# Optimization experiments

Hardware: AMD Instinct MI355X
Metric: run time of the kernel (lower is better)

Reference implementation:

```python
import jax, jax.numpy as jnp
import numpy as np

PRESERVE_RATIO = 0.8
TEMPERATURE = 1.5


def setup_inputs() -> dict:
    key = jax.random.key(0)
    ks = jax.random.split(key, 8)
    B, C, H, W = 2, 64, 96, 96
    inter = C // 2
    bott = C // 4
    s = 0.02
    return {
        "x": jax.random.normal(ks[0], (B, C, H, W), dtype=jnp.float32),
        "g_w": jax.random.normal(ks[1], (inter, C), dtype=jnp.float32) * s,
        "theta_w": jax.random.normal(ks[2], (inter, C), dtype=jnp.float32) * s,
        "phi_w": jax.random.normal(ks[3], (inter, C), dtype=jnp.float32) * s,
        "W_w": jax.random.normal(ks[4], (C, inter), dtype=jnp.float32) * s,
        "cg1_w": jax.random.normal(ks[5], (bott, C), dtype=jnp.float32) * s,
        "cg1_b": jnp.zeros((bott,), dtype=jnp.float32),
        "cg2_w": jax.random.normal(ks[6], (C, bott), dtype=jnp.float32) * s,
        "cg2_b": jnp.zeros((C,), dtype=jnp.float32),
    }


def reference(x, g_w, theta_w, phi_w, W_w, cg1_w, cg1_b, cg2_w, cg2_b):
    B, C, H, W = x.shape
    N = H * W
    # color gate: global avg pool -> 1x1 conv -> relu -> 1x1 conv -> sigmoid
    pooled = jnp.mean(x, axis=(2, 3))                       # [B, C]
    h = jax.nn.relu(pooled @ cg1_w.T + cg1_b)               # [B, C//4]
    gate = jax.nn.sigmoid(h @ cg2_w.T + cg2_b)              # [B, C]

    xf = x.reshape(B, C, N)                                 # [B, C, N]
    g_x = jnp.einsum('ic,bcn->bni', g_w, xf)                # [B, N, I]
    theta = jnp.einsum('ic,bcn->bni', theta_w, xf)          # [B, N, I]
    phi = jnp.einsum('ic,bcn->bin', phi_w, xf)              # [B, I, N]

    affinity = jnp.einsum('bni,bim->bnm', theta, phi) / TEMPERATURE  # [B, N, N]
    affinity = jax.nn.softmax(affinity, axis=-1)
    y = jnp.einsum('bnm,bmi->bni', affinity, g_x)           # [B, N, I]
    y = jnp.einsum('ci,bni->bcn', W_w, y).reshape(B, C, H, W)
    y = y * gate[:, :, None, None] * PRESERVE_RATIO
    return x + y
```

## Files before the change

kernel.cpp:

```cpp
#include <hip/hip_runtime.h>

#define N_TOK 9216
#define C_DIM 64
#define I_DIM 32
#define BOT 16
#define B_SZ 2
#define N_TILES 144

typedef short bf16x8 __attribute__((ext_vector_type(8)));
typedef float f32x4 __attribute__((ext_vector_type(4)));
typedef float f32x16 __attribute__((ext_vector_type(16)));

__device__ __forceinline__ unsigned packbf(float a, float b) {
  return __builtin_amdgcn_perm(__float_as_uint(b), __float_as_uint(a), 0x07060302u);
}
__device__ __forceinline__ unsigned short bftrunc(float f) {
  return (unsigned short)(__float_as_uint(f) >> 16);
}

__global__ __launch_bounds__(256) void pool_kernel(const float* __restrict__ x,
                                                   float* __restrict__ pooled) {
  int bc = blockIdx.x;
  const float* p = x + (size_t)bc * N_TOK;
  float s = 0.f;
  for (int t = threadIdx.x; t < N_TOK; t += 256) s += p[t];
#pragma unroll
  for (int off = 32; off >= 1; off >>= 1) s += __shfl_down(s, off, 64);
  __shared__ float red[4];
  int wid = threadIdx.x >> 6, lane = threadIdx.x & 63;
  if (lane == 0) red[wid] = s;
  __syncthreads();
  if (threadIdx.x == 0)
    pooled[bc] = (red[0] + red[1] + red[2] + red[3]) * (1.0f / N_TOK);
}

__global__ __launch_bounds__(256) void proj_kernel(
    const float* __restrict__ x, const float* __restrict__ g_w,
    const float* __restrict__ theta_w, const float* __restrict__ phi_w,
    unsigned short* __restrict__ Q, unsigned short* __restrict__ K,
    unsigned short* __restrict__ VT) {
  const int lane = threadIdx.x & 63;
  const int m = lane & 15, quad = lane >> 4;
  int task = blockIdx.x * 4 + (threadIdx.x >> 6);
  int mat = task / 1152;
  int r0 = task % 1152;
  int b = r0 / 576;
  int n0 = (r0 % 576) * 16;
  const float* wsrc = (mat == 0) ? theta_w : ((mat == 1) ? phi_w : g_w);
  const float scale = (mat == 0) ? 0.96179669439f : 1.0f;

  bf16x8 afr[2][2];
#pragma unroll
  for (int it = 0; it < 2; ++it)
#pragma unroll
    for (int cs = 0; cs < 2; ++cs) {
      const float* wp = wsrc + (it * 16 + m) * C_DIM + cs * 32 + quad * 8;
      union { unsigned u[4]; bf16x8 v; } t;
#pragma unroll
      for (int j = 0; j < 4; ++j)
        t.u[j] = packbf(wp[2 * j] * scale, wp[2 * j + 1] * scale);
      afr[it][cs] = t.v;
    }

  const float* xb = x + (size_t)b * C_DIM * N_TOK + n0 + m;
  bf16x8 bfr[2];
#pragma unroll
  for (int cs = 0; cs < 2; ++cs) {
    union { unsigned u[4]; bf16x8 v; } t;
#pragma unroll
    for (int j = 0; j < 4; ++j) {
      float v0 = xb[(size_t)(cs * 32 + quad * 8 + 2 * j) * N_TOK];
      float v1 = xb[(size_t)(cs * 32 + quad * 8 + 2 * j + 1) * N_TOK];
      t.u[j] = packbf(v0, v1);
    }
    bfr[cs] = t.v;
  }

  f32x4 acc[2] = {{0.f, 0.f, 0.f, 0.f}, {0.f, 0.f, 0.f, 0.f}};
#pragma unroll
  for (int cs = 0; cs < 2; ++cs)
#pragma unroll
    for (int it = 0; it < 2; ++it)
      acc[it] = __builtin_amdgcn_mfma_f32_16x16x32_bf16(afr[it][cs], bfr[cs],
                                                        acc[it], 0, 0, 0);
  if (mat < 2) {
    unsigned short* dst =
        ((mat == 0) ? Q : K) + ((size_t)b * N_TOK + n0 + m) * I_DIM;
#pragma unroll
    for (int it = 0; it < 2; ++it) {
      unsigned u0 = packbf(acc[it][0], acc[it][1]);
      unsigned u1 = packbf(acc[it][2], acc[it][3]);
      *(uint2*)(dst + it * 16 + quad * 4) = make_uint2(u0, u1);
    }
  } else {
#pragma unroll
    for (int it = 0; it < 2; ++it)
#pragma unroll
      for (int r = 0; r < 4; ++r)
        VT[((size_t)b * I_DIM + it * 16 + quad * 4 + r) * N_TOK + n0 + m] =
            bftrunc(acc[it][r]);
  }
}

__global__ __launch_bounds__(256, 4) void attn_kernel(
    const unsigned short* __restrict__ Q, const unsigned short* __restrict__ Kg,
    const unsigned short* __restrict__ VT, float* __restrict__ Ypart,
    float* __restrict__ Lpart, int tps) {
  const int lane = threadIdx.x & 63;
  const int l32 = lane & 31, h = lane >> 5;
  const int wid = threadIdx.x >> 6;
  const int qw = blockIdx.x * 4 + wid;
  const int ks = blockIdx.y, b = blockIdx.z;
  const int q0 = qw * 32;
  const unsigned short* Qb = Q + (size_t)b * N_TOK * I_DIM;
  const unsigned short* Kb = Kg + (size_t)b * N_TOK * I_DIM;
  const unsigned short* Vb = VT + (size_t)b * I_DIM * N_TOK;

  __shared__ __align__(16) unsigned short Pw[4][32][68];
  unsigned short(*P)[68] = Pw[wid];

  bf16x8 bq0 = *(const bf16x8*)(Qb + (size_t)(q0 + l32) * I_DIM + h * 8);
  bf16x8 bq1 = *(const bf16x8*)(Qb + (size_t)(q0 + l32) * I_DIM + 16 + h * 8);

  const f32x16 zz = {};
  f32x16 accy = {};
  float lsum = 0.f;

  const int kt0 = ks * tps;
  for (int kt = kt0; kt < kt0 + tps; ++kt) {
    const int k0 = kt * 64;
    const unsigned short* kp = Kb + (size_t)(k0 + l32) * I_DIM + h * 8;
    bf16x8 ak00 = *(const bf16x8*)(kp);
    bf16x8 ak01 = *(const bf16x8*)(kp + 16);
    bf16x8 ak10 = *(const bf16x8*)(kp + 32 * I_DIM);
    bf16x8 ak11 = *(const bf16x8*)(kp + 32 * I_DIM + 16);
    const unsigned short* vp = Vb + (size_t)l32 * N_TOK + k0 + h * 8;
    bf16x8 bv[4];
    bv[0] = *(const bf16x8*)(vp);
    bv[1] = *(const bf16x8*)(vp + 16);
    bv[2] = *(const bf16x8*)(vp + 32);
    bv[3] = *(const bf16x8*)(vp + 48);

    f32x16 s0 = __builtin_amdgcn_mfma_f32_32x32x16_bf16(ak00, bq0, zz, 0, 0, 0);
    s0 = __builtin_amdgcn_mfma_f32_32x32x16_bf16(ak01, bq1, s0, 0, 0, 0);
    f32x16 s1 = __builtin_amdgcn_mfma_f32_32x32x16_bf16(ak10, bq0, zz, 0, 0, 0);
    s1 = __builtin_amdgcn_mfma_f32_32x32x16_bf16(ak11, bq1, s1, 0, 0, 0);

#pragma unroll
    for (int t = 0; t < 2; ++t) {
      const f32x16 sv = t ? s1 : s0;
      float e[16];
#pragma unroll
      for (int r = 0; r < 16; ++r) {
        e[r] = __builtin_amdgcn_exp2f(sv[r]);
        lsum += e[r];
      }
      unsigned pk[8];
#pragma unroll
      for (int i = 0; i < 8; ++i) pk[i] = packbf(e[2 * i], e[2 * i + 1]);
      unsigned short* row = &P[l32][t * 32 + 4 * h];
      *(uint2*)(row) = make_uint2(pk[0], pk[1]);
      *(uint2*)(row + 8) = make_uint2(pk[2], pk[3]);
      *(uint2*)(row + 16) = make_uint2(pk[4], pk[5]);
      *(uint2*)(row + 24) = make_uint2(pk[6], pk[7]);
    }

#pragma unroll
    for (int s = 0; s < 4; ++s) {
      union { uint2 d[2]; bf16x8 v; } ap;
      const unsigned short* rp = &P[l32][16 * s + 8 * h];
      ap.d[0] = *(const uint2*)(rp);
      ap.d[1] = *(const uint2*)(rp + 4);
      accy = __builtin_amdgcn_mfma_f32_32x32x16_bf16(ap.v, bv[s], accy, 0, 0, 0);
    }
  }

  lsum += __shfl_xor(lsum, 32, 64);

  const size_t base = (size_t)(ks * B_SZ + b) * N_TOK + q0;
#pragma unroll
  for (int R = 0; R < 4; ++R)
#pragma unroll
    for (int r = 0; r < 4; ++r)
      Ypart[(base + r + 8 * R + 4 * h) * I_DIM + l32] = accy[4 * R + r];
  if (h == 0) Lpart[base + l32] = lsum;
}

__global__ __launch_bounds__(256) void epilogue_kernel(
    const float* __restrict__ x, const float* __restrict__ W_w,
    const float* __restrict__ pooled, const float* __restrict__ cg1_w,
    const float* __restrict__ cg1_b, const float* __restrict__ cg2_w,
    const float* __restrict__ cg2_b, const float* __restrict__ Ypart,
    const float* __restrict__ Lpart, float* __restrict__ out, int KS) {
  __shared__ float Ysh[64][33];
  __shared__ float lsh[64];
  __shared__ float gsh[64];
  __shared__ float hl[BOT];
  const int t = threadIdx.x;
  const int b = blockIdx.y;
  const int n0 = blockIdx.x * 64;

  if (t < BOT) {
    float a = cg1_b[t];
#pragma unroll
    for (int c = 0; c < C_DIM; ++c)
      a += cg1_w[t * C_DIM + c] * pooled[b * C_DIM + c];
    hl[t] = a > 0.f ? a : 0.f;
  }

  {
    int nl = t >> 2, i0 = (t & 3) * 8;
    float4 s0 = make_float4(0.f, 0.f, 0.f, 0.f), s1 = s0;
    for (int ks = 0; ks < KS; ++ks) {
      const float* yp =
          Ypart + ((size_t)(ks * B_SZ + b) * N_TOK + n0 + nl) * I_DIM + i0;
      float4 v0 = *(const float4*)(yp);
      float4 v1 = *(const float4*)(yp + 4);
      s0.x += v0.x; s0.y += v0.y; s0.z += v0.z; s0.w += v0.w;
      s1.x += v1.x; s1.y += v1.y; s1.z += v1.z; s1.w += v1.w;
    }
    Ysh[nl][i0 + 0] = s0.x; Ysh[nl][i0 + 1] = s0.y;
    Ysh[nl][i0 + 2] = s0.z; Ysh[nl][i0 + 3] = s0.w;
    Ysh[nl][i0 + 4] = s1.x; Ysh[nl][i0 + 5] = s1.y;
    Ysh[nl][i0 + 6] = s1.z; Ysh[nl][i0 + 7] = s1.w;
    if (t < 64) {
      float ls = 0.f;
      for (int ks = 0; ks < KS; ++ks)
        ls += Lpart[(size_t)(ks * B_SZ + b) * N_TOK + n0 + t];
      lsh[t] = ls;
    }
  }
  __syncthreads();

  if (t < C_DIM) {
    float z = cg2_b[t];
#pragma unroll
    for (int j = 0; j < BOT; ++j) z += cg2_w[t * BOT + j] * hl[j];
    gsh[t] = 0.8f / (1.f + __expf(-z));
  }
  __syncthreads();

  const int n = t & 63, cg = t >> 6;
  float y[I_DIM];
#pragma unroll
  for (int i = 0; i < I_DIM; ++i) y[i] = Ysh[n][i];
  const float inv = 1.0f / lsh[n];
  const float* xb = x + ((size_t)b * C_DIM + cg * 16) * N_TOK + n0 + n;
  float* ob = out + ((size_t)b * C_DIM + cg * 16) * N_TOK + n0 + n;
#pragma unroll
  for (int c16 = 0; c16 < 16; ++c16) {
    const int c = cg * 16 + c16;
    float sacc = 0.f;
#pragma unroll
    for (int i = 0; i < I_DIM; ++i) sacc += W_w[c * I_DIM + i] * y[i];
    ob[(size_t)c16 * N_TOK] = xb[(size_t)c16 * N_TOK] + gsh[c] * inv * sacc;
  }
}

extern "C" void kernel_launch(void* const* d_in, const int* in_sizes, int n_in,
                              void* d_out, int out_size, void* d_ws, size_t ws_size,
                              hipStream_t stream) {
  const float* x = (const float*)d_in[0];
  const float* g_w = (const float*)d_in[1];
  const float* theta_w = (const float*)d_in[2];
  const float* phi_w = (const float*)d_in[3];
  const float* W_w = (const float*)d_in[4];
  const float* cg1_w = (const float*)d_in[5];
  const float* cg1_b = (const float*)d_in[6];
  const float* cg2_w = (const float*)d_in[7];
  const float* cg2_b = (const float*)d_in[8];
  float* out = (float*)d_out;

  char* w = (char*)d_ws;
  const size_t bfsz = (size_t)B_SZ * N_TOK * I_DIM * sizeof(unsigned short);
  unsigned short* Qb = (unsigned short*)(w);
  unsigned short* Kb = (unsigned short*)(w + bfsz);
  unsigned short* VT = (unsigned short*)(w + 2 * bfsz);
  float* pooled = (float*)(w + 3 * bfsz);
  char* w2 = w + 3 * bfsz + 1024;

  int KS = 8;
  {
    const size_t per = (size_t)B_SZ * N_TOK * sizeof(float) * (I_DIM + 1);
    while (KS > 1 && (3 * bfsz + 1024 + (size_t)KS * per) > ws_size) KS >>= 1;
  }
  float* Lpart = (float*)w2;
  float* Ypart = (float*)(w2 + (size_t)KS * B_SZ * N_TOK * sizeof(float));
  int tps = N_TILES / KS;

  proj_kernel<<<dim3(864), 256, 0, stream>>>(x, g_w, theta_w, phi_w, Qb, Kb, VT);
  pool_kernel<<<dim3(B_SZ * C_DIM), 256, 0, stream>>>(x, pooled);
  attn_kernel<<<dim3(72, KS, B_SZ), 256, 0, stream>>>(Qb, Kb, VT, Ypart, Lpart, tps);
  epilogue_kernel<<<dim3(N_TOK / 64, B_SZ), 256, 0, stream>>>(
      x, W_w, pooled, cg1_w, cg1_b, cg2_w, cg2_b, Ypart, Lpart, out, KS);
}
```

Before: 173.6 us.

## Fuse pooling into projection, raise split-K and occupancy, transpose Ypart layout

Merges the pooling kernel into the projection kernel as extra blocks, which removes one launch. Raises attention occupancy hints from 4 to 8 waves and the key split from 8 to 16 for more parallelism. Splits the softmax row-sum into two accumulators to shorten the dependency chain. Stores partial outputs as [I][N] with float4 writes, and the epilogue transposes them through shared memory. The costs are register pressure that may force spills, double the partial-sum traffic in the epilogue, and possible shared-memory bank conflicts on the transposed writes.

After: 219.0 us. +26.1%, slower.

```diff
diff --git a/kernel.cpp b/kernel.cpp
--- a/kernel.cpp
+++ b/kernel.cpp
@@ -18,27 +18,26 @@
   return (unsigned short)(__float_as_uint(f) >> 16);
 }
 
-__global__ __launch_bounds__(256) void pool_kernel(const float* __restrict__ x,
-                                                   float* __restrict__ pooled) {
-  int bc = blockIdx.x;
-  const float* p = x + (size_t)bc * N_TOK;
-  float s = 0.f;
-  for (int t = threadIdx.x; t < N_TOK; t += 256) s += p[t];
-#pragma unroll
-  for (int off = 32; off >= 1; off >>= 1) s += __shfl_down(s, off, 64);
-  __shared__ float red[4];
-  int wid = threadIdx.x >> 6, lane = threadIdx.x & 63;
-  if (lane == 0) red[wid] = s;
-  __syncthreads();
-  if (threadIdx.x == 0)
-    pooled[bc] = (red[0] + red[1] + red[2] + red[3]) * (1.0f / N_TOK);
-}
-
-__global__ __launch_bounds__(256) void proj_kernel(
+__global__ __launch_bounds__(256) void proj_pool_kernel(
     const float* __restrict__ x, const float* __restrict__ g_w,
     const float* __restrict__ theta_w, const float* __restrict__ phi_w,
     unsigned short* __restrict__ Q, unsigned short* __restrict__ K,
-    unsigned short* __restrict__ VT) {
+    unsigned short* __restrict__ VT, float* __restrict__ pooled) {
+  if (blockIdx.x >= 864) {
+    int bc = blockIdx.x - 864;
+    const float* p = x + (size_t)bc * N_TOK;
+    float s = 0.f;
+    for (int t = threadIdx.x; t < N_TOK; t += 256) s += p[t];
+#pragma unroll
+    for (int off = 32; off >= 1; off >>= 1) s += __shfl_down(s, off, 64);
+    __shared__ float red[4];
+    int wid = threadIdx.x >> 6, lane = threadIdx.x & 63;
+    if (lane == 0) red[wid] = s;
+    __syncthreads();
+    if (threadIdx.x == 0)
+      pooled[bc] = (red[0] + red[1] + red[2] + red[3]) * (1.0f / N_TOK);
+    return;
+  }
   const int lane = threadIdx.x & 63;
   const int m = lane & 15, quad = lane >> 4;
   int task = blockIdx.x * 4 + (threadIdx.x >> 6);
@@ -102,7 +101,7 @@
   }
 }
 
-__global__ __launch_bounds__(256, 4) void attn_kernel(
+__global__ __launch_bounds__(256, 8) void attn_kernel(
     const unsigned short* __restrict__ Q, const unsigned short* __restrict__ Kg,
     const unsigned short* __restrict__ VT, float* __restrict__ Ypart,
     float* __restrict__ Lpart, int tps) {
@@ -146,14 +145,17 @@
     f32x16 s1 = __builtin_amdgcn_mfma_f32_32x32x16_bf16(ak10, bq0, zz, 0, 0, 0);
     s1 = __builtin_amdgcn_mfma_f32_32x32x16_bf16(ak11, bq1, s1, 0, 0, 0);
 
+    float2 ls2 = make_float2(0.f, 0.f);
 #pragma unroll
     for (int t = 0; t < 2; ++t) {
       const f32x16 sv = t ? s1 : s0;
       float e[16];
 #pragma unroll
-      for (int r = 0; r < 16; ++r) {
-        e[r] = __builtin_amdgcn_exp2f(sv[r]);
-        lsum += e[r];
+      for (int r = 0; r < 16; ++r) e[r] = __builtin_amdgcn_exp2f(sv[r]);
+#pragma unroll
+      for (int r = 0; r < 8; ++r) {
+        ls2.x += e[2 * r];
+        ls2.y += e[2 * r + 1];
       }
       unsigned pk[8];
 #pragma unroll
@@ -164,6 +166,7 @@
       *(uint2*)(row + 16) = make_uint2(pk[4], pk[5]);
       *(uint2*)(row + 24) = make_uint2(pk[6], pk[7]);
     }
+    lsum += ls2.x + ls2.y;
 
 #pragma unroll
     for (int s = 0; s < 4; ++s) {
@@ -177,13 +180,14 @@
 
   lsum += __shfl_xor(lsum, 32, 64);
 
-  const size_t base = (size_t)(ks * B_SZ + b) * N_TOK + q0;
-#pragma unroll
-  for (int R = 0; R < 4; ++R)
-#pragma unroll
-    for (int r = 0; r < 4; ++r)
-      Ypart[(base + r + 8 * R + 4 * h) * I_DIM + l32] = accy[4 * R + r];
-  if (h == 0) Lpart[base + l32] = lsum;
+  const size_t ib = ((size_t)(ks * B_SZ + b) * I_DIM + l32) * N_TOK + q0 + 4 * h;
+#pragma unroll
+  for (int R = 0; R < 4; ++R) {
+    float4 v = make_float4(accy[4 * R], accy[4 * R + 1], accy[4 * R + 2],
+                           accy[4 * R + 3]);
+    *(float4*)(Ypart + ib + 8 * R) = v;
+  }
+  if (h == 0) Lpart[(size_t)(ks * B_SZ + b) * N_TOK + q0 + l32] = lsum;
 }
 
 __global__ __launch_bounds__(256) void epilogue_kernel(
@@ -209,20 +213,20 @@
   }
 
   {
-    int nl = t >> 2, i0 = (t & 3) * 8;
-    float4 s0 = make_float4(0.f, 0.f, 0.f, 0.f), s1 = s0;
+    int i = t >> 3, ns = (t & 7) * 8;
+    float4 a0 = make_float4(0.f, 0.f, 0.f, 0.f), a1 = a0;
     for (int ks = 0; ks < KS; ++ks) {
       const float* yp =
-          Ypart + ((size_t)(ks * B_SZ + b) * N_TOK + n0 + nl) * I_DIM + i0;
+          Ypart + ((size_t)(ks * B_SZ + b) * I_DIM + i) * N_TOK + n0 + ns;
       float4 v0 = *(const float4*)(yp);
       float4 v1 = *(const float4*)(yp + 4);
-      s0.x += v0.x; s0.y += v0.y; s0.z += v0.z; s0.w += v0.w;
-      s1.x += v1.x; s1.y += v1.y; s1.z += v1.z; s1.w += v1.w;
-    }
-    Ysh[nl][i0 + 0] = s0.x; Ysh[nl][i0 + 1] = s0.y;
-    Ysh[nl][i0 + 2] = s0.z; Ysh[nl][i0 + 3] = s0.w;
-    Ysh[nl][i0 + 4] = s1.x; Ysh[nl][i0 + 5] = s1.y;
-    Ysh[nl][i0 + 6] = s1.z; Ysh[nl][i0 + 7] = s1.w;
+      a0.x += v0.x; a0.y += v0.y; a0.z += v0.z; a0.w += v0.w;
+      a1.x += v1.x; a1.y += v1.y; a1.z += v1.z; a1.w += v1.w;
+    }
+    Ysh[ns + 0][i] = a0.x; Ysh[ns + 1][i] = a0.y;
+    Ysh[ns + 2][i] = a0.z; Ysh[ns + 3][i] = a0.w;
+    Ysh[ns + 4][i] = a1.x; Ysh[ns + 5][i] = a1.y;
+    Ysh[ns + 6][i] = a1.z; Ysh[ns + 7][i] = a1.w;
     if (t < 64) {
       float ls = 0.f;
       for (int ks = 0; ks < KS; ++ks)
@@ -279,7 +283,7 @@
   float* pooled = (float*)(w + 3 * bfsz);
   char* w2 = w + 3 * bfsz + 1024;
 
-  int KS = 8;
+  int KS = 16;
   {
     const size_t per = (size_t)B_SZ * N_TOK * sizeof(float) * (I_DIM + 1);
     while (KS > 1 && (3 * bfsz + 1024 + (size_t)KS * per) > ws_size) KS >>= 1;
@@ -288,8 +292,8 @@
   float* Ypart = (float*)(w2 + (size_t)KS * B_SZ * N_TOK * sizeof(float));
   int tps = N_TILES / KS;
 
-  proj_kernel<<<dim3(864), 256, 0, stream>>>(x, g_w, theta_w, phi_w, Qb, Kb, VT);
-  pool_kernel<<<dim3(B_SZ * C_DIM), 256, 0, stream>>>(x, pooled);
+  proj_pool_kernel<<<dim3(992), 256, 0, stream>>>(x, g_w, theta_w, phi_w, Qb,
+                                                  Kb, VT, pooled);
   attn_kernel<<<dim3(72, KS, B_SZ), 256, 0, stream>>>(Qb, Kb, VT, Ypart, Lpart, tps);
   epilogue_kernel<<<dim3(N_TOK / 64, B_SZ), 256, 0, stream>>>(
       x, W_w, pooled, cg1_w, cg1_b, cg2_w, cg2_b, Ypart, Lpart, out, KS);
```
